# Optimization experiments

Hardware: AMD Instinct MI355X
Metric: run time of the kernel (lower is better)

Reference implementation:

```python
import jax, jax.numpy as jnp
import numpy as np

B, T, D, H = 4, 2048, 1024, 64

def setup_inputs() -> dict:
    key = jax.random.key(0)
    kx, kq, kk, kv = jax.random.split(key, 4)
    s = 1.0 / np.sqrt(D)
    return {
        "x": jax.random.normal(kx, (B, T, D), dtype=jnp.float32),
        "Wq": jax.random.normal(kq, (D, H), dtype=jnp.float32) * s,
        "Wk": jax.random.normal(kk, (D, H), dtype=jnp.float32) * s,
        "Wv": jax.random.normal(kv, (D, H), dtype=jnp.float32) * s,
    }

def reference(x, Wq, Wk, Wv):
    # q,k,v: [B,T,H]
    q = jnp.einsum('btd,dh->bth', x, Wq)
    k = jnp.einsum('btd,dh->bth', x, Wk)
    v = jnp.einsum('btd,dh->bth', x, Wv)
    scale = jnp.asarray(H, x.dtype) ** -0.5
    wei = jnp.einsum('bqh,bkh->bqk', q, k) * scale  # [B,T,T]
    Tlen = x.shape[1]
    causal = jnp.tril(jnp.ones((Tlen, Tlen), dtype=bool))
    wei = jnp.where(causal, wei, -jnp.inf)
    attn = jax.nn.softmax(wei, axis=-1)
    return jnp.einsum('bqk,bkh->bqh', attn, v)
```

## Files before the change

kernel.cpp:

```cpp
#include <hip/hip_runtime.h>
#include <hip/hip_bf16.h>
#include <math.h>

#define Bb   4
#define Tlen 2048
#define Dd   1024
#define Hh   64
#define NROWS 8192
#define NQ   32
#define NC   4

typedef short bf16x8 __attribute__((ext_vector_type(8)));
typedef float f32x4  __attribute__((ext_vector_type(4)));

__device__ __forceinline__ unsigned short f2b(float f) {
    unsigned u = __float_as_uint(f);
    unsigned r = u + 0x7FFFu + ((u >> 16) & 1u);
    return (unsigned short)(r >> 16);
}
__device__ __forceinline__ unsigned pk2(float a, float b) {
    __hip_bfloat162 h = __float22bfloat162_rn(make_float2(a, b));
    return *reinterpret_cast<unsigned*>(&h);
}

__global__ __launch_bounds__(256) void wtrans_kernel(
    const float* __restrict__ Wq, const float* __restrict__ Wk,
    const float* __restrict__ Wv, unsigned short* __restrict__ wfrag)
{
    const int s = blockIdx.x * 256 + threadIdx.x;
    const int f   = s / 768;
    const int rem = s % 768;
    const int nb  = rem >> 6;
    const int lane = rem & 63;
    const int g = lane >> 4, qr = lane & 15;
    const int n = nb * 16 + qr;
    const int wsel = n >> 6, h = n & 63;
    const float* W = (wsel == 0) ? Wq : (wsel == 1) ? Wk : Wv;
    const int k0 = (f >> 1) * 64 + (f & 1) * 32 + g * 8;
    unsigned short tmp[8];
    #pragma unroll
    for (int j = 0; j < 8; ++j) tmp[j] = f2b(W[(size_t)(k0 + j) * Hh + h]);
    *(bf16x8*)(wfrag + (size_t)s * 8) = *(const bf16x8*)tmp;
}

__global__ __launch_bounds__(256) void proj_kernel(
    const float* __restrict__ x, const unsigned short* __restrict__ wfrag,
    unsigned short* __restrict__ qw, unsigned short* __restrict__ kw,
    unsigned short* __restrict__ vw)
{
    __shared__ unsigned short xs[2][32 * 64];

    const int rb   = blockIdx.x * 32;
    const int tid  = threadIdx.x;
    const int wv   = tid >> 6;
    const int lane = tid & 63;
    const int qr   = lane & 15;
    const int g    = lane >> 4;

    const int xr = tid >> 3, xc8 = tid & 7;
    const float* xg0 = x + (size_t)(rb + xr) * Dd + xc8 * 8;

    const unsigned short* wp = wfrag + ((size_t)(wv * 3) * 64 + lane) * 8;

    f32x4 acc[6] = {};

    float4 px0 = *(const float4*)(xg0 + 0);
    float4 px1 = *(const float4*)(xg0 + 4);

    bf16x8 wr[6];
    #pragma unroll
    for (int ks = 0; ks < 2; ++ks)
        #pragma unroll
        for (int nf = 0; nf < 3; ++nf)
            wr[ks * 3 + nf] = *(const bf16x8*)(wp + (size_t)(ks * 12 + nf) * 512);

    #pragma unroll
    for (int t = 0; t < 16; ++t) {
        const int cur = t & 1;
        {
            union { unsigned u[4]; bf16x8 v; } p8;
            p8.u[0] = pk2(px0.x, px0.y);
            p8.u[1] = pk2(px0.z, px0.w);
            p8.u[2] = pk2(px1.x, px1.y);
            p8.u[3] = pk2(px1.z, px1.w);
            *(bf16x8*)(&xs[cur][xr * 64 + ((xc8 ^ (xr & 7)) << 3)]) = p8.v;
        }
        __syncthreads();

        bf16x8 wn[6];
        if (t < 15) {
            px0 = *(const float4*)(xg0 + (t + 1) * 64 + 0);
            px1 = *(const float4*)(xg0 + (t + 1) * 64 + 4);
            const int fb = (t + 1) * 2;
            #pragma unroll
            for (int ks = 0; ks < 2; ++ks)
                #pragma unroll
                for (int nf = 0; nf < 3; ++nf)
                    wn[ks * 3 + nf] = *(const bf16x8*)(wp + (size_t)((fb + ks) * 12 + nf) * 512);
        }

        #pragma unroll
        for (int ks = 0; ks < 2; ++ks) {
            #pragma unroll
            for (int mf = 0; mf < 2; ++mf) {
                const int arow = mf * 16 + qr;
                const bf16x8 a = *(const bf16x8*)(
                    &xs[cur][arow * 64 + (((ks * 4 + g) ^ (arow & 7)) << 3)]);
                acc[mf * 3 + 0] = __builtin_amdgcn_mfma_f32_16x16x32_bf16(a, wr[ks * 3 + 0], acc[mf * 3 + 0], 0, 0, 0);
                acc[mf * 3 + 1] = __builtin_amdgcn_mfma_f32_16x16x32_bf16(a, wr[ks * 3 + 1], acc[mf * 3 + 1], 0, 0, 0);
                acc[mf * 3 + 2] = __builtin_amdgcn_mfma_f32_16x16x32_bf16(a, wr[ks * 3 + 2], acc[mf * 3 + 2], 0, 0, 0);
            }
        }
        __syncthreads();

        if (t < 15) {
            #pragma unroll
            for (int i = 0; i < 6; ++i) wr[i] = wn[i];
        }
    }

    #pragma unroll
    for (int mf = 0; mf < 2; ++mf) {
        #pragma unroll
        for (int nf = 0; nf < 3; ++nf) {
            const int n = wv * 48 + nf * 16 + qr;
            const int wsel = n >> 6, h = n & 63;
            unsigned short* out = (wsel == 0) ? qw : (wsel == 1) ? kw : vw;
            const f32x4 ov = acc[mf * 3 + nf];
            #pragma unroll
            for (int r = 0; r < 4; ++r)
                out[(size_t)(rb + mf * 16 + 4 * g + r) * Hh + h] = f2b(ov[r]);
        }
    }
}

#define XSTR 72
#define VSTR 40
__global__ __launch_bounds__(256) void attn_kernel(
    const unsigned short* __restrict__ qw, const unsigned short* __restrict__ kw,
    const unsigned short* __restrict__ vw,
    float* __restrict__ part_O, float* __restrict__ part_ml)
{
    __shared__ unsigned short ks_s[32 * XSTR];
    __shared__ unsigned short vt_s[64 * VSTR];

    const int qt = (NQ - 1) - blockIdx.x;
    const int ci = blockIdx.y;
    const int b  = blockIdx.z;
    const int tid = threadIdx.x;
    const int wv = tid >> 6, lane = tid & 63;
    const int qr = lane & 15, g = lane >> 4;

    const int ntk = 2 * qt + 2;
    const int tpc = (ntk + NC - 1) / NC;
    const int t0  = ci * tpc;
    const int t1  = (ntk < t0 + tpc) ? ntk : (t0 + tpc);

    const size_t base = (size_t)b * Tlen * Hh;
    const int qrow = qt * 64 + wv * 16 + qr;

    const bf16x8 qf0 = *(const bf16x8*)(qw + base + (size_t)qrow * Hh + 8 * g);
    const bf16x8 qf1 = *(const bf16x8*)(qw + base + (size_t)qrow * Hh + 32 + 8 * g);

    f32x4 o0 = {}, o1 = {}, o2 = {}, o3 = {};
    float m = -INFINITY, l = 0.f;

    const int srow = tid >> 3, scg = tid & 7;
    const unsigned short* kbase = kw + base + (size_t)srow * Hh + scg * 8;
    const unsigned short* vbase = vw + base + (size_t)srow * Hh + scg * 8;
    const int ksw = ((scg ^ (srow & 3)) << 3);
    bf16x8 k8 = {}, v8 = {};
    if (t0 < t1) {
        k8 = *(const bf16x8*)(kbase + (size_t)t0 * 32 * Hh);
        v8 = *(const bf16x8*)(vbase + (size_t)t0 * 32 * Hh);
    }

    for (int kt = t0; kt < t1; ++kt) {
        const int j0 = kt * 32;
        __syncthreads();
        {
            *(bf16x8*)(&ks_s[srow * XSTR + ksw]) = k8;
            #pragma unroll
            for (int u = 0; u < 8; ++u) {
                const int c = scg * 8 + u;
                const int jx = srow ^ (((c >> 3) & 3) << 3);
                vt_s[c * VSTR + jx] = ((const unsigned short*)&v8)[u];
            }
        }
        __syncthreads();

        if (kt + 1 < t1) {
            k8 = *(const bf16x8*)(kbase + (size_t)(kt + 1) * 32 * Hh);
            v8 = *(const bf16x8*)(vbase + (size_t)(kt + 1) * 32 * Hh);
        }

        f32x4 a0 = {}, a1 = {};
        {
            const int sw = (g ^ (qr & 3)) << 3;
            bf16x8 kf;
            kf = *(const bf16x8*)(&ks_s[qr * XSTR + sw]);
            a0 = __builtin_amdgcn_mfma_f32_16x16x32_bf16(kf, qf0, a0, 0, 0, 0);
            kf = *(const bf16x8*)(&ks_s[qr * XSTR + 32 + sw]);
            a0 = __builtin_amdgcn_mfma_f32_16x16x32_bf16(kf, qf1, a0, 0, 0, 0);
            kf = *(const bf16x8*)(&ks_s[(16 + qr) * XSTR + sw]);
            a1 = __builtin_amdgcn_mfma_f32_16x16x32_bf16(kf, qf0, a1, 0, 0, 0);
            kf = *(const bf16x8*)(&ks_s[(16 + qr) * XSTR + 32 + sw]);
            a1 = __builtin_amdgcn_mfma_f32_16x16x32_bf16(kf, qf1, a1, 0, 0, 0);
        }

        float p[8];
        float tm = -INFINITY;
        #pragma unroll
        for (int jf = 0; jf < 2; ++jf) {
            #pragma unroll
            for (int r = 0; r < 4; ++r) {
                const int jg = j0 + jf * 16 + 4 * g + r;
                float s = ((jf == 0) ? a0[r] : a1[r]) * 0.125f;
                s = (jg > qrow) ? -INFINITY : s;
                p[jf * 4 + r] = s;
                tm = fmaxf(tm, s);
            }
        }
        tm = fmaxf(tm, __shfl_xor(tm, 16));
        tm = fmaxf(tm, __shfl_xor(tm, 32));
        const float mnew = fmaxf(m, tm);
        const float mc   = fmaxf(mnew, -1e30f);
        float psum = 0.f;
        #pragma unroll
        for (int i = 0; i < 8; ++i) {
            const float pv = __expf(p[i] - mc);
            p[i] = pv; psum += pv;
        }
        psum += __shfl_xor(psum, 16);
        psum += __shfl_xor(psum, 32);

        if (!__all(tm <= m)) {
            const float alpha = (m == -INFINITY) ? 0.f : __expf(m - mc);
            const float ar0 = __shfl(alpha, 4 * g + 0);
            const float ar1 = __shfl(alpha, 4 * g + 1);
            const float ar2 = __shfl(alpha, 4 * g + 2);
            const float ar3 = __shfl(alpha, 4 * g + 3);
            o0[0] *= ar0; o0[1] *= ar1; o0[2] *= ar2; o0[3] *= ar3;
            o1[0] *= ar0; o1[1] *= ar1; o1[2] *= ar2; o1[3] *= ar3;
            o2[0] *= ar0; o2[1] *= ar1; o2[2] *= ar2; o2[3] *= ar3;
            o3[0] *= ar0; o3[1] *= ar1; o3[2] *= ar2; o3[3] *= ar3;
            l = l * alpha + psum;
        } else {
            l += psum;
        }
        m = mnew;

        unsigned pw[4];
        pw[0] = f2b(p[0]) | ((unsigned)f2b(p[1]) << 16);
        pw[1] = f2b(p[2]) | ((unsigned)f2b(p[3]) << 16);
        pw[2] = f2b(p[4]) | ((unsigned)f2b(p[5]) << 16);
        pw[3] = f2b(p[6]) | ((unsigned)f2b(p[7]) << 16);
        union PU { unsigned u[4]; bf16x8 v; } pu;
        #pragma unroll
        for (int w = 0; w < 4; ++w) {
            const int gp  = 2 * g + (w >> 1);
            const int src = 16 * (gp & 3) + qr;
            const unsigned t0s = __shfl(pw[0 + (w & 1)], src);
            const unsigned t1s = __shfl(pw[2 + (w & 1)], src);
            pu.u[w] = (gp & 4) ? t1s : t0s;
        }
        const bf16x8 pa = pu.v;

        {
            int cb = qr;
            bf16x8 vf = *(const bf16x8*)(&vt_s[cb * VSTR + 8 * (g ^ ((cb >> 3) & 3))]);
            o0 = __builtin_amdgcn_mfma_f32_16x16x32_bf16(pa, vf, o0, 0, 0, 0);
            cb = 16 + qr;
            vf = *(const bf16x8*)(&vt_s[cb * VSTR + 8 * (g ^ ((cb >> 3) & 3))]);
            o1 = __builtin_amdgcn_mfma_f32_16x16x32_bf16(pa, vf, o1, 0, 0, 0);
            cb = 32 + qr;
            vf = *(const bf16x8*)(&vt_s[cb * VSTR + 8 * (g ^ ((cb >> 3) & 3))]);
            o2 = __builtin_amdgcn_mfma_f32_16x16x32_bf16(pa, vf, o2, 0, 0, 0);
            cb = 48 + qr;
            vf = *(const bf16x8*)(&vt_s[cb * VSTR + 8 * (g ^ ((cb >> 3) & 3))]);
            o3 = __builtin_amdgcn_mfma_f32_16x16x32_bf16(pa, vf, o3, 0, 0, 0);
        }
    }

    const int blin = (b * NQ + qt) * NC + ci;
    float* po = part_O + (size_t)blin * 4096;
    #pragma unroll
    for (int nf = 0; nf < 4; ++nf) {
        const f32x4 ov = (nf == 0) ? o0 : (nf == 1) ? o1 : (nf == 2) ? o2 : o3;
        #pragma unroll
        for (int r = 0; r < 4; ++r)
            po[(size_t)(wv * 16 + 4 * g + r) * 64 + nf * 16 + qr] = ov[r];
    }
    if (g == 0) {
        part_ml[(size_t)blin * 128 + wv * 16 + qr]      = m;
        part_ml[(size_t)blin * 128 + 64 + wv * 16 + qr] = l;
    }
}

__global__ __launch_bounds__(256) void merge_kernel(
    const float* __restrict__ part_O, const float* __restrict__ part_ml,
    float* __restrict__ out)
{
    const int idx = blockIdx.x * 256 + threadIdx.x;
    const int row = idx >> 6;
    const int c   = idx & 63;
    const int b   = row >> 11;
    const int t   = row & 2047;
    const int qt  = t >> 6;
    const int qq  = t & 63;
    const int bl0 = (b * NQ + qt) * NC;

    float M = -INFINITY;
    #pragma unroll
    for (int i = 0; i < NC; ++i) {
        const float lvi = part_ml[(size_t)(bl0 + i) * 128 + 64 + qq];
        if (lvi > 0.f) M = fmaxf(M, part_ml[(size_t)(bl0 + i) * 128 + qq]);
    }
    float num = 0.f, den = 0.f;
    #pragma unroll
    for (int i = 0; i < NC; ++i) {
        const float lvi = part_ml[(size_t)(bl0 + i) * 128 + 64 + qq];
        if (lvi > 0.f) {
            const float wgt = __expf(part_ml[(size_t)(bl0 + i) * 128 + qq] - M);
            num += wgt * part_O[(size_t)(bl0 + i) * 4096 + (size_t)qq * 64 + c];
            den += wgt * lvi;
        }
    }
    out[(size_t)row * 64 + c] = num / den;
}

extern "C" void kernel_launch(void* const* d_in, const int* in_sizes, int n_in,
                              void* d_out, int out_size, void* d_ws, size_t ws_size,
                              hipStream_t stream) {
    const float* x  = (const float*)d_in[0];
    const float* Wq = (const float*)d_in[1];
    const float* Wk = (const float*)d_in[2];
    const float* Wv = (const float*)d_in[3];
    float* outp = (float*)d_out;

    unsigned short* wfrag = (unsigned short*)d_ws;
    unsigned short* qw = wfrag + 192 * 1024;
    unsigned short* kw = qw + NROWS * Hh;
    unsigned short* vw = kw + NROWS * Hh;
    float* part_O  = (float*)(vw + NROWS * Hh);
    float* part_ml = part_O + (size_t)(Bb * NQ * NC) * 4096;

    wtrans_kernel<<<dim3(96), 256, 0, stream>>>(Wq, Wk, Wv, wfrag);
    proj_kernel<<<dim3(NROWS / 32), 256, 0, stream>>>(x, wfrag, qw, kw, vw);
    attn_kernel<<<dim3(NQ, NC, Bb), 256, 0, stream>>>(qw, kw, vw, part_O, part_ml);
    merge_kernel<<<dim3((NROWS * Hh) / 256), 256, 0, stream>>>(part_O, part_ml, outp);
}
```

Baseline: 48.52 us.

## Store V transposed in projection and load K/V fragments directly from global

The projection kernel now writes V in a per-batch transposed [H,T] layout. The attention kernel drops its shared-memory staging of K and V, so the two barriers per tile and the scalar V transpose go away. Each wave instead loads its MFMA fragments for K and V straight from global memory into registers, prefetching the next tile. The cost is redundant global/L2 traffic, since all four waves fetch the same K/V fragments. The transposed V stores from the projection kernel are also strided and uncoalesced.

```diff
diff --git a/kernel.cpp b/kernel.cpp
--- a/kernel.cpp
+++ b/kernel.cpp
@@ -46,7 +46,7 @@
 __global__ __launch_bounds__(256) void proj_kernel(
     const float* __restrict__ x, const unsigned short* __restrict__ wfrag,
     unsigned short* __restrict__ qw, unsigned short* __restrict__ kw,
-    unsigned short* __restrict__ vw)
+    unsigned short* __restrict__ vwT)
 {
     __shared__ unsigned short xs[2][32 * 64];
 
@@ -125,25 +125,26 @@
         for (int nf = 0; nf < 3; ++nf) {
             const int n = wv * 48 + nf * 16 + qr;
             const int wsel = n >> 6, h = n & 63;
-            unsigned short* out = (wsel == 0) ? qw : (wsel == 1) ? kw : vw;
             const f32x4 ov = acc[mf * 3 + nf];
             #pragma unroll
-            for (int r = 0; r < 4; ++r)
-                out[(size_t)(rb + mf * 16 + 4 * g + r) * Hh + h] = f2b(ov[r]);
-        }
-    }
-}
-
-#define XSTR 72
-#define VSTR 40
+            for (int r = 0; r < 4; ++r) {
+                const int row = rb + mf * 16 + 4 * g + r;
+                if (wsel == 2) {
+                    vwT[((size_t)(row >> 11) * Hh + h) * Tlen + (row & 2047)] = f2b(ov[r]);
+                } else {
+                    unsigned short* out = (wsel == 0) ? qw : kw;
+                    out[(size_t)row * Hh + h] = f2b(ov[r]);
+                }
+            }
+        }
+    }
+}
+
 __global__ __launch_bounds__(256) void attn_kernel(
     const unsigned short* __restrict__ qw, const unsigned short* __restrict__ kw,
-    const unsigned short* __restrict__ vw,
+    const unsigned short* __restrict__ vwT,
     float* __restrict__ part_O, float* __restrict__ part_ml)
 {
-    __shared__ unsigned short ks_s[32 * XSTR];
-    __shared__ unsigned short vt_s[64 * VSTR];
-
     const int qt = (NQ - 1) - blockIdx.x;
     const int ci = blockIdx.y;
     const int b  = blockIdx.z;
@@ -157,6 +158,8 @@
     const int t1  = (ntk < t0 + tpc) ? ntk : (t0 + tpc);
 
     const size_t base = (size_t)b * Tlen * Hh;
+    const unsigned short* kwb = kw + base;
+    const unsigned short* vtb = vwT + (size_t)b * Hh * Tlen;
     const int qrow = qt * 64 + wv * 16 + qr;
 
     const bf16x8 qf0 = *(const bf16x8*)(qw + base + (size_t)qrow * Hh + 8 * g);
@@ -165,48 +168,43 @@
     f32x4 o0 = {}, o1 = {}, o2 = {}, o3 = {};
     float m = -INFINITY, l = 0.f;
 
-    const int srow = tid >> 3, scg = tid & 7;
-    const unsigned short* kbase = kw + base + (size_t)srow * Hh + scg * 8;
-    const unsigned short* vbase = vw + base + (size_t)srow * Hh + scg * 8;
-    const int ksw = ((scg ^ (srow & 3)) << 3);
-    bf16x8 k8 = {}, v8 = {};
+    const size_t kO = (size_t)qr * 64 + g * 8;
+    const size_t vO = (size_t)qr * 2048 + g * 8;
+
+    bf16x8 kf[4], vf[4];
     if (t0 < t1) {
-        k8 = *(const bf16x8*)(kbase + (size_t)t0 * 32 * Hh);
-        v8 = *(const bf16x8*)(vbase + (size_t)t0 * 32 * Hh);
+        const size_t j64 = (size_t)t0 * 32 * 64;
+        kf[0] = *(const bf16x8*)(kwb + j64 + kO);
+        kf[1] = *(const bf16x8*)(kwb + j64 + kO + 32);
+        kf[2] = *(const bf16x8*)(kwb + j64 + kO + 16 * 64);
+        kf[3] = *(const bf16x8*)(kwb + j64 + kO + 16 * 64 + 32);
+        vf[0] = *(const bf16x8*)(vtb + vO + t0 * 32);
+        vf[1] = *(const bf16x8*)(vtb + vO + 16 * 2048 + t0 * 32);
+        vf[2] = *(const bf16x8*)(vtb + vO + 32 * 2048 + t0 * 32);
+        vf[3] = *(const bf16x8*)(vtb + vO + 48 * 2048 + t0 * 32);
     }
 
     for (int kt = t0; kt < t1; ++kt) {
         const int j0 = kt * 32;
-        __syncthreads();
-        {
-            *(bf16x8*)(&ks_s[srow * XSTR + ksw]) = k8;
-            #pragma unroll
-            for (int u = 0; u < 8; ++u) {
-                const int c = scg * 8 + u;
-                const int jx = srow ^ (((c >> 3) & 3) << 3);
-                vt_s[c * VSTR + jx] = ((const unsigned short*)&v8)[u];
-            }
-        }
-        __syncthreads();
-
+
+        bf16x8 kn[4], vn[4];
         if (kt + 1 < t1) {
-            k8 = *(const bf16x8*)(kbase + (size_t)(kt + 1) * 32 * Hh);
-            v8 = *(const bf16x8*)(vbase + (size_t)(kt + 1) * 32 * Hh);
+            const size_t j64 = (size_t)(kt + 1) * 32 * 64;
+            kn[0] = *(const bf16x8*)(kwb + j64 + kO);
+            kn[1] = *(const bf16x8*)(kwb + j64 + kO + 32);
+            kn[2] = *(const bf16x8*)(kwb + j64 + kO + 16 * 64);
+            kn[3] = *(const bf16x8*)(kwb + j64 + kO + 16 * 64 + 32);
+            vn[0] = *(const bf16x8*)(vtb + vO + (kt + 1) * 32);
+            vn[1] = *(const bf16x8*)(vtb + vO + 16 * 2048 + (kt + 1) * 32);
+            vn[2] = *(const bf16x8*)(vtb + vO + 32 * 2048 + (kt + 1) * 32);
+            vn[3] = *(const bf16x8*)(vtb + vO + 48 * 2048 + (kt + 1) * 32);
         }
 
         f32x4 a0 = {}, a1 = {};
-        {
-            const int sw = (g ^ (qr & 3)) << 3;
-            bf16x8 kf;
-            kf = *(const bf16x8*)(&ks_s[qr * XSTR + sw]);
-            a0 = __builtin_amdgcn_mfma_f32_16x16x32_bf16(kf, qf0, a0, 0, 0, 0);
-            kf = *(const bf16x8*)(&ks_s[qr * XSTR + 32 + sw]);
-            a0 = __builtin_amdgcn_mfma_f32_16x16x32_bf16(kf, qf1, a0, 0, 0, 0);
-            kf = *(const bf16x8*)(&ks_s[(16 + qr) * XSTR + sw]);
-            a1 = __builtin_amdgcn_mfma_f32_16x16x32_bf16(kf, qf0, a1, 0, 0, 0);
-            kf = *(const bf16x8*)(&ks_s[(16 + qr) * XSTR + 32 + sw]);
-            a1 = __builtin_amdgcn_mfma_f32_16x16x32_bf16(kf, qf1, a1, 0, 0, 0);
-        }
+        a0 = __builtin_amdgcn_mfma_f32_16x16x32_bf16(kf[0], qf0, a0, 0, 0, 0);
+        a0 = __builtin_amdgcn_mfma_f32_16x16x32_bf16(kf[1], qf1, a0, 0, 0, 0);
+        a1 = __builtin_amdgcn_mfma_f32_16x16x32_bf16(kf[2], qf0, a1, 0, 0, 0);
+        a1 = __builtin_amdgcn_mfma_f32_16x16x32_bf16(kf[3], qf1, a1, 0, 0, 0);
 
         float p[8];
         float tm = -INFINITY;
@@ -266,19 +264,14 @@
         }
         const bf16x8 pa = pu.v;
 
-        {
-            int cb = qr;
-            bf16x8 vf = *(const bf16x8*)(&vt_s[cb * VSTR + 8 * (g ^ ((cb >> 3) & 3))]);
-            o0 = __builtin_amdgcn_mfma_f32_16x16x32_bf16(pa, vf, o0, 0, 0, 0);
-            cb = 16 + qr;
-            vf = *(const bf16x8*)(&vt_s[cb * VSTR + 8 * (g ^ ((cb >> 3) & 3))]);
-            o1 = __builtin_amdgcn_mfma_f32_16x16x32_bf16(pa, vf, o1, 0, 0, 0);
-            cb = 32 + qr;
-            vf = *(const bf16x8*)(&vt_s[cb * VSTR + 8 * (g ^ ((cb >> 3) & 3))]);
-            o2 = __builtin_amdgcn_mfma_f32_16x16x32_bf16(pa, vf, o2, 0, 0, 0);
-            cb = 48 + qr;
-            vf = *(const bf16x8*)(&vt_s[cb * VSTR + 8 * (g ^ ((cb >> 3) & 3))]);
-            o3 = __builtin_amdgcn_mfma_f32_16x16x32_bf16(pa, vf, o3, 0, 0, 0);
+        o0 = __builtin_amdgcn_mfma_f32_16x16x32_bf16(pa, vf[0], o0, 0, 0, 0);
+        o1 = __builtin_amdgcn_mfma_f32_16x16x32_bf16(pa, vf[1], o1, 0, 0, 0);
+        o2 = __builtin_amdgcn_mfma_f32_16x16x32_bf16(pa, vf[2], o2, 0, 0, 0);
+        o3 = __builtin_amdgcn_mfma_f32_16x16x32_bf16(pa, vf[3], o3, 0, 0, 0);
+
+        if (kt + 1 < t1) {
+            #pragma unroll
+            for (int i = 0; i < 4; ++i) { kf[i] = kn[i]; vf[i] = vn[i]; }
         }
     }
 
@@ -339,14 +332,14 @@
     float* outp = (float*)d_out;
 
     unsigned short* wfrag = (unsigned short*)d_ws;
-    unsigned short* qw = wfrag + 192 * 1024;
-    unsigned short* kw = qw + NROWS * Hh;
-    unsigned short* vw = kw + NROWS * Hh;
-    float* part_O  = (float*)(vw + NROWS * Hh);
+    unsigned short* qw  = wfrag + 192 * 1024;
+    unsigned short* kw  = qw + NROWS * Hh;
+    unsigned short* vwT = kw + NROWS * Hh;
+    float* part_O  = (float*)(vwT + NROWS * Hh);
     float* part_ml = part_O + (size_t)(Bb * NQ * NC) * 4096;
 
     wtrans_kernel<<<dim3(96), 256, 0, stream>>>(Wq, Wk, Wv, wfrag);
-    proj_kernel<<<dim3(NROWS / 32), 256, 0, stream>>>(x, wfrag, qw, kw, vw);
-    attn_kernel<<<dim3(NQ, NC, Bb), 256, 0, stream>>>(qw, kw, vw, part_O, part_ml);
+    proj_kernel<<<dim3(NROWS / 32), 256, 0, stream>>>(x, wfrag, qw, kw, vwT);
+    attn_kernel<<<dim3(NQ, NC, Bb), 256, 0, stream>>>(qw, kw, vwT, part_O, part_ml);
     merge_kernel<<<dim3((NROWS * Hh) / 256), 256, 0, stream>>>(part_O, part_ml, outp);
 }
```

New measurement: 60.81 us. +25.3%, slower.
